# Performance work log

Hardware: AMD Instinct MI355X
Metric: run time of the kernel (lower is better)

The kernel has to match this reference:

```python
import jax, jax.numpy as jnp
import numpy as np

N_NODES = 100000
N_EDGES = 1600000
D_IN = 128
D_HID = 128
D_OUT = 10
N_GRAPHS = 512


def _sage_conv(x, src, dst, W_l, b_l, W_r, num_nodes):
    # PyG SAGEConv (mean aggr): out = lin_l(mean_{j in N(i)} x_j) + lin_r(x_i)
    msg = x[src]                                            # [E, D] gather
    s = jax.ops.segment_sum(msg, dst, num_segments=num_nodes)
    cnt = jax.ops.segment_sum(jnp.ones((src.shape[0], 1), x.dtype), dst,
                              num_segments=num_nodes)
    mean = s / jnp.maximum(cnt, 1.0)                        # 0 where no neighbors
    return mean @ W_l.T + b_l + x @ W_r.T


def setup_inputs() -> dict:
    key = jax.random.key(0)
    ks = jax.random.split(key, 10)
    glorot = lambda k, o, i: jax.random.normal(k, (o, i), jnp.float32) * (1.0 / np.sqrt(i))
    return {
        "x": jax.random.normal(ks[0], (N_NODES, D_IN), jnp.float32),
        "edge_index": jax.random.randint(ks[1], (2, N_EDGES), 0, N_NODES, jnp.int64),
        "batch": jnp.sort(jax.random.randint(ks[2], (N_NODES,), 0, N_GRAPHS, jnp.int64)),
        "W1_l": glorot(ks[3], D_HID, D_IN),
        "b1": jnp.zeros((D_HID,), jnp.float32),
        "W1_r": glorot(ks[4], D_HID, D_IN),
        "W2_l": glorot(ks[5], D_HID, D_HID),
        "b2": jnp.zeros((D_HID,), jnp.float32),
        "W2_r": glorot(ks[6], D_HID, D_HID),
        "Wf": glorot(ks[7], D_OUT, D_HID),
        "bf": jnp.zeros((D_OUT,), jnp.float32),
    }


def reference(x, edge_index, batch, W1_l, b1, W1_r, W2_l, b2, W2_r, Wf, bf):
    src, dst = edge_index[0], edge_index[1]
    n = x.shape[0]
    h = jax.nn.relu(_sage_conv(x, src, dst, W1_l, b1, W1_r, n))
    h = jax.nn.relu(_sage_conv(h, src, dst, W2_l, b2, W2_r, n))
    # global_mean_pool over graph ids
    gsum = jax.ops.segment_sum(h, batch, num_segments=N_GRAPHS)
    gcnt = jax.ops.segment_sum(jnp.ones((n, 1), h.dtype), batch, num_segments=N_GRAPHS)
    g = gsum / jnp.maximum(gcnt, 1.0)
    logits = g @ Wf.T + bf
    return jax.nn.log_softmax(logits, axis=-1)
```

## Files before the change

### kernel.cpp

```cpp
#include <hip/hip_runtime.h>
#include <hip/hip_bf16.h>

#define N_NODES 100000
#define N_EDGES 1600000
#define N_GRAPHS 512
#define NB 256
#define NPB 391
#define CHUNK 6250
#define STAGE 7680

typedef __attribute__((ext_vector_type(8))) short short8;
typedef __attribute__((ext_vector_type(4))) float f32x4;
typedef __attribute__((ext_vector_type(2))) float f32x2;

__device__ __forceinline__ float b2f(ushort u) {
    union { unsigned int i; float f; } c; c.i = ((unsigned int)u) << 16; return c.f;
}
__device__ __forceinline__ float blo(unsigned int u) {
    union { unsigned int i; float f; } c; c.i = u << 16; return c.f;
}
__device__ __forceinline__ float bhi(unsigned int u) {
    union { unsigned int i; float f; } c; c.i = u & 0xffff0000u; return c.f;
}
__device__ __forceinline__ ushort f2b(float f) {
    union { float f; unsigned int i; } c; c.f = f;
    unsigned int r = (c.i + 0x7fffu + ((c.i >> 16) & 1u)) >> 16;
    return (ushort)r;
}
__device__ __forceinline__ int idx_at(const void* p, long i, int f) {
    return f ? (int)((const long long*)p)[i] : ((const int*)p)[i];
}
__device__ __forceinline__ short8 dec8(const uchar* p) {
    uint2 q = *(const uint2*)p;
    f32x2 d0 = __builtin_amdgcn_cvt_pk_f32_fp8((int)q.x, false);
    f32x2 d1 = __builtin_amdgcn_cvt_pk_f32_fp8((int)q.x, true);
    f32x2 d2 = __builtin_amdgcn_cvt_pk_f32_fp8((int)q.y, false);
    f32x2 d3 = __builtin_amdgcn_cvt_pk_f32_fp8((int)q.y, true);
    short8 s;
    s[0] = (short)f2b(d0.x); s[1] = (short)f2b(d0.y);
    s[2] = (short)f2b(d1.x); s[3] = (short)f2b(d1.y);
    s[4] = (short)f2b(d2.x); s[5] = (short)f2b(d2.y);
    s[6] = (short)f2b(d3.x); s[7] = (short)f2b(d3.y);
    return s;
}

__global__ __launch_bounds__(256) void k_detect(const unsigned int* __restrict__ xw,
                                                const unsigned int* __restrict__ ew,
                                                const int* __restrict__ bw,
                                                int* __restrict__ flags) {
    __shared__ int cf, ce, cb;
    int t = threadIdx.x;
    if (t == 0) { cf = 0; ce = 0; cb = 0; }
    __syncthreads();
    unsigned int w = xw[t];
    unsigned int e = (w >> 7) & 0xffu;
    if (e >= 110u && e <= 130u) atomicAdd(&cf, 1);
    if (t < 128) {
        if (ew[2 * t + 1] != 0u) atomicAdd(&ce, 1);
        if (bw[99001 + 2 * t] != 0) atomicAdd(&cb, 1);
    }
    __syncthreads();
    if (t == 0) {
        flags[0] = (cf >= 128) ? 1 : 0;
        flags[1] = (ce == 0) ? 1 : 0;
        flags[2] = (cb == 0) ? 1 : 0;
    }
}

__global__ __launch_bounds__(256) void k_prep(const void* __restrict__ ei,
                                              const void* __restrict__ x,
                                              ushort* __restrict__ xbf,
                                              unsigned int* __restrict__ xf8,
                                              const void* W1l, const void* W1r,
                                              const void* W2l, const void* W2r,
                                              const void* b1,  const void* b2,
                                              ushort* __restrict__ wbf,
                                              int* __restrict__ blkcnt,
                                              const int* __restrict__ flags) {
    int b = blockIdx.x, t = threadIdx.x;
    if (b < NB) {
        __shared__ int h[NB];
        int f = flags[1];
        for (int j = t; j < NB; j += 256) h[j] = 0;
        __syncthreads();
        int lo = b * CHUNK, hi = lo + CHUNK;
        for (int e = lo + t; e < hi; e += 256) {
            int d = idx_at(ei, (long)N_EDGES + e, f);
            atomicAdd(&h[d / NPB], 1);
        }
        __syncthreads();
        if (t < NB) blkcnt[b * NB + t] = h[t];
    } else if (b < NB + 2048) {
        bool f32src = (flags[0] == 0);
        int vb = b - NB;
        const long nG = (long)N_NODES * 128 / 4;
        for (long g = (long)vb * 256 + t; g < nG; g += 2048L * 256) {
            float v0, v1, v2, v3;
            if (f32src) {
                float4 vv = ((const float4*)x)[g];
                v0 = vv.x; v1 = vv.y; v2 = vv.z; v3 = vv.w;
                unsigned int lo = (unsigned int)f2b(v0) | ((unsigned int)f2b(v1) << 16);
                unsigned int hi = (unsigned int)f2b(v2) | ((unsigned int)f2b(v3) << 16);
                ((uint2*)xbf)[g] = make_uint2(lo, hi);
            } else {
                uint2 q = ((const uint2*)x)[g];
                v0 = blo(q.x); v1 = bhi(q.x); v2 = blo(q.y); v3 = bhi(q.y);
            }
            int r = __builtin_amdgcn_cvt_pk_fp8_f32(v0, v1, 0, false);
            r = __builtin_amdgcn_cvt_pk_fp8_f32(v2, v3, r, true);
            xf8[g] = (unsigned int)r;
        }
    } else {
        int idx = (b - NB - 2048) * 256 + t;
        if (idx >= 65792) return;
        const void* src; int off;
        if      (idx < 16384) { src = W1l; off = idx; }
        else if (idx < 32768) { src = W1r; off = idx - 16384; }
        else if (idx < 49152) { src = W2l; off = idx - 32768; }
        else if (idx < 65536) { src = W2r; off = idx - 49152; }
        else if (idx < 65664) { src = b1;  off = idx - 65536; }
        else                  { src = b2;  off = idx - 65664; }
        wbf[idx] = (flags[0] != 0) ? ((const ushort*)src)[off]
                                   : f2b(((const float*)src)[off]);
    }
}

__global__ __launch_bounds__(NB) void k_bscan(const int* __restrict__ blkcnt,
                                              int* __restrict__ bucketBase,
                                              int* __restrict__ blkbase) {
    __shared__ int s[NB];
    int t = threadIdx.x;
    int tot = 0;
    for (int blk = 0; blk < NB; ++blk) tot += blkcnt[blk * NB + t];
    s[t] = tot; __syncthreads();
    for (int off = 1; off < NB; off <<= 1) {
        int a = (t >= off) ? s[t - off] : 0;
        __syncthreads();
        s[t] += a;
        __syncthreads();
    }
    int excl = s[t] - tot;
    bucketBase[t] = excl;
    if (t == NB - 1) bucketBase[NB] = s[NB - 1];
    int run = excl;
    for (int blk = 0; blk < NB; ++blk) {
        blkbase[blk * NB + t] = run;
        run += blkcnt[blk * NB + t];
    }
}

__global__ __launch_bounds__(256) void k_bin(const void* __restrict__ ei,
                                             const int* __restrict__ blkbase,
                                             int* __restrict__ binned,
                                             const int* __restrict__ flags) {
    __shared__ int bb[NB];
    __shared__ int rank[NB];
    int t = threadIdx.x, blk = blockIdx.x;
    int f = flags[1];
    for (int j = t; j < NB; j += 256) { bb[j] = blkbase[blk * NB + j]; rank[j] = 0; }
    __syncthreads();
    int lo = blk * CHUNK, hi = lo + CHUNK;
    for (int e = lo + t; e < hi; e += 256) {
        int s = idx_at(ei, e, f);
        int d = idx_at(ei, (long)N_EDGES + e, f);
        int b = d / NPB;
        int loc = d - b * NPB;
        int r = atomicAdd(&rank[b], 1);
        binned[bb[b] + r] = s | (loc << 20);
    }
}

__global__ __launch_bounds__(256) void k_csr(const int* __restrict__ binned,
                                             const int* __restrict__ bucketBase,
                                             int* __restrict__ rowptr,
                                             int* __restrict__ csr) {
    __shared__ int cnt[400];
    __shared__ int sc[400];
    __shared__ int sh[256];
    __shared__ int stage[STAGE];
    int t = threadIdx.x, b = blockIdx.x;
    int nodeLo = b * NPB;
    int nC = N_NODES - nodeLo; if (nC > NPB) nC = NPB;
    int eBase = bucketBase[b], eEnd = bucketBase[b + 1];

    for (int j = t; j < 400; j += 256) cnt[j] = 0;
    __syncthreads();
    for (int i = eBase + t; i < eEnd; i += 256)
        atomicAdd(&cnt[binned[i] >> 20], 1);
    __syncthreads();
    int base = t * 2;
    int v0 = (base < 400) ? cnt[base] : 0;
    int v1 = (base + 1 < 400) ? cnt[base + 1] : 0;
    int ssum = v0 + v1;
    sh[t] = ssum; __syncthreads();
    for (int off = 1; off < 256; off <<= 1) {
        int a = (t >= off) ? sh[t - off] : 0;
        __syncthreads();
        sh[t] += a;
        __syncthreads();
    }
    int pre = sh[t] - ssum;
    if (base < 400) sc[base] = pre;
    if (base + 1 < 400) sc[base + 1] = pre + v0;
    __syncthreads();
    for (int j = t; j < nC; j += 256) rowptr[nodeLo + j] = eBase + sc[j];
    if (b == NB - 1) {
        if (t == 0) rowptr[N_NODES] = eEnd;
        if (t < 64) csr[N_EDGES + t] = 0;
    }
    for (int j = t; j < 400; j += 256) cnt[j] = 0;
    __syncthreads();
    for (int i = eBase + t; i < eEnd; i += 256) {
        int p = binned[i];
        int loc = p >> 20;
        int pos = sc[loc] + atomicAdd(&cnt[loc], 1);
        int srcn = p & 0xFFFFF;
        if (pos < STAGE) stage[pos] = srcn;
        else csr[eBase + pos] = srcn;
    }
    __syncthreads();
    int eCnt = eEnd - eBase; if (eCnt > STAGE) eCnt = STAGE;
    for (int j = t; j < eCnt; j += 256) csr[eBase + j] = stage[j];
}

__global__ __launch_bounds__(256) void k_agg(const uint4* __restrict__ x8,
                                             const int* __restrict__ rowptr,
                                             const int* __restrict__ csr,
                                             uint4* __restrict__ mout) {
    int wv = blockIdx.x * 4 + (threadIdx.x >> 6);
    int lane = threadIdx.x & 63;
    int li = lane & 7;
    int node = wv * 8 + (lane >> 3);
    int beg = rowptr[node];
    int end = rowptr[node + 1];
    int deg = end - beg;
    int m = deg;
    m = max(m, __shfl_xor(m, 8));
    m = max(m, __shfl_xor(m, 16));
    m = max(m, __shfl_xor(m, 32));
    int degmax = __builtin_amdgcn_readfirstlane(m);
    float a[16];
#pragma unroll
    for (int i = 0; i < 16; ++i) a[i] = 0.f;
    for (int j = 0; j < degmax; j += 8) {
        int pos = beg + j + li;
        if (pos > end - 1) pos = (deg > 0) ? end - 1 : 0;
        int vidx = csr[pos];
        uint4 p[8];
#pragma unroll
        for (int i = 0; i < 8; ++i) {
            int idx = __shfl(vidx, i | (lane & 56));
            p[i] = x8[(long)idx * 8 + li];
        }
#pragma unroll
        for (int i = 0; i < 8; ++i) {
            bool ok = (j + i < deg);
            unsigned int q0 = ok ? p[i].x : 0u;
            unsigned int q1 = ok ? p[i].y : 0u;
            unsigned int q2 = ok ? p[i].z : 0u;
            unsigned int q3 = ok ? p[i].w : 0u;
            f32x2 d;
            d = __builtin_amdgcn_cvt_pk_f32_fp8((int)q0, false); a[0] += d.x;  a[1] += d.y;
            d = __builtin_amdgcn_cvt_pk_f32_fp8((int)q0, true);  a[2] += d.x;  a[3] += d.y;
            d = __builtin_amdgcn_cvt_pk_f32_fp8((int)q1, false); a[4] += d.x;  a[5] += d.y;
            d = __builtin_amdgcn_cvt_pk_f32_fp8((int)q1, true);  a[6] += d.x;  a[7] += d.y;
            d = __builtin_amdgcn_cvt_pk_f32_fp8((int)q2, false); a[8] += d.x;  a[9] += d.y;
            d = __builtin_amdgcn_cvt_pk_f32_fp8((int)q2, true);  a[10] += d.x; a[11] += d.y;
            d = __builtin_amdgcn_cvt_pk_f32_fp8((int)q3, false); a[12] += d.x; a[13] += d.y;
            d = __builtin_amdgcn_cvt_pk_f32_fp8((int)q3, true);  a[14] += d.x; a[15] += d.y;
        }
    }
    float s = (deg > 0) ? 1.f / (float)deg : 0.f;
    uint4 o;
    int r;
    r = __builtin_amdgcn_cvt_pk_fp8_f32(a[0] * s, a[1] * s, 0, false);
    r = __builtin_amdgcn_cvt_pk_fp8_f32(a[2] * s, a[3] * s, r, true);  o.x = (unsigned int)r;
    r = __builtin_amdgcn_cvt_pk_fp8_f32(a[4] * s, a[5] * s, 0, false);
    r = __builtin_amdgcn_cvt_pk_fp8_f32(a[6] * s, a[7] * s, r, true);  o.y = (unsigned int)r;
    r = __builtin_amdgcn_cvt_pk_fp8_f32(a[8] * s, a[9] * s, 0, false);
    r = __builtin_amdgcn_cvt_pk_fp8_f32(a[10] * s, a[11] * s, r, true); o.z = (unsigned int)r;
    r = __builtin_amdgcn_cvt_pk_fp8_f32(a[12] * s, a[13] * s, 0, false);
    r = __builtin_amdgcn_cvt_pk_fp8_f32(a[14] * s, a[15] * s, r, true); o.w = (unsigned int)r;
    mout[(long)node * 8 + li] = o;
}

__global__ __launch_bounds__(256) void k_gemm(const uchar* __restrict__ A0f8,
                                              const ushort* __restrict__ A1a,
                                              const ushort* __restrict__ A1b,
                                              const uchar* __restrict__ A1f8,
                                              const ushort* __restrict__ Wl,
                                              const ushort* __restrict__ Wr,
                                              const ushort* __restrict__ bias,
                                              ushort* __restrict__ outb,
                                              uchar* __restrict__ out8,
                                              const int* __restrict__ flags,
                                              int layer1) {
    __shared__ short Ws[4096 * 8];
    int t = threadIdx.x;
    const ushort* A1 = flags[0] ? A1a : A1b;
#pragma unroll
    for (int i = 0; i < 16; ++i) {
        int f = i * 256 + t;
        int lane = f & 63, kk = (f >> 6) & 7, tile = f >> 9;
        int o = tile * 16 + (lane & 15);
        int k0 = kk * 32 + ((lane >> 4) * 8);
        const ushort* wsrc = (k0 < 128) ? (Wl + o * 128 + k0)
                                        : (Wr + o * 128 + (k0 - 128));
        *(short8*)&Ws[f * 8] = *(const short8*)wsrc;
    }
    __syncthreads();

    int wid = t >> 6, lane = t & 63;
    long nbase = (long)blockIdx.x * 64 + (long)wid * 16;
    int arow = (int)nbase + (lane & 15);
    if (arow >= N_NODES) arow = N_NODES - 1;
    int kq = (lane >> 4) * 8;

    short8 afrag[8];
#pragma unroll
    for (int kk = 0; kk < 8; ++kk) {
        int k0 = kk * 32 + kq;
        if (k0 < 128) {
            afrag[kk] = dec8(A0f8 + (long)arow * 128 + k0);
        } else if (layer1) {
            afrag[kk] = *(const short8*)(A1 + (long)arow * 128 + (k0 - 128));
        } else {
            afrag[kk] = dec8(A1f8 + (long)arow * 128 + (k0 - 128));
        }
    }

#pragma unroll
    for (int tile = 0; tile < 8; ++tile) {
        f32x4 acc = {0.f, 0.f, 0.f, 0.f};
#pragma unroll
        for (int kk = 0; kk < 8; ++kk) {
            short8 bfrag = *(short8*)&Ws[((tile * 8 + kk) * 64 + lane) * 8];
            acc = __builtin_amdgcn_mfma_f32_16x16x32_bf16(afrag[kk], bfrag, acc, 0, 0, 0);
        }
        int o = tile * 16 + (lane & 15);
        float bo = b2f(bias[o]);
#pragma unroll
        for (int r = 0; r < 4; ++r) {
            long node = nbase + (lane >> 4) * 4 + r;
            if (node < N_NODES) {
                float v = acc[r] + bo;
                v = v > 0.f ? v : 0.f;
                if (layer1) {
                    int pp = __builtin_amdgcn_cvt_pk_fp8_f32(v, v, 0, false);
                    out8[node * 128 + o] = (uchar)pp;
                } else {
                    outb[node * 128 + o] = f2b(v);
                }
            }
        }
    }
}

__global__ __launch_bounds__(256) void k_pool_cls(const ushort* __restrict__ h2,
                                                  const void* __restrict__ batch,
                                                  const void* __restrict__ Wf,
                                                  const void* __restrict__ bfv,
                                                  void* __restrict__ outp,
                                                  const int* __restrict__ flags) {
    int g = blockIdx.x, t = threadIdx.x;
    int wid = t >> 6, lane = t & 63;
    bool f32 = (flags[0] == 0);
    int b64 = flags[2];
    __shared__ int rng[2];
    __shared__ float redA[4][64];
    __shared__ float redB[4][64];
    __shared__ float gv[128];
    __shared__ float lg[10];
    if (t < 2) {
        int v = g + t, lo = 0, hi = N_NODES;
        while (lo < hi) {
            int mid = (lo + hi) >> 1;
            if (idx_at(batch, mid, b64) < v) lo = mid + 1; else hi = mid;
        }
        rng[t] = lo;
    }
    __syncthreads();
    int lo = rng[0], hi = rng[1];
    const unsigned int* xr = (const unsigned int*)h2;
    float a0 = 0.f, a1 = 0.f;
    int n = lo + wid;
    for (; n + 28 < hi; n += 32) {
        unsigned int p[8];
#pragma unroll
        for (int i = 0; i < 8; ++i) p[i] = xr[(long)(n + i * 4) * 64 + lane];
#pragma unroll
        for (int i = 0; i < 8; ++i) { a0 += blo(p[i]); a1 += bhi(p[i]); }
    }
    for (; n < hi; n += 4) {
        unsigned int q = xr[(long)n * 64 + lane];
        a0 += blo(q); a1 += bhi(q);
    }
    redA[wid][lane] = a0;
    redB[wid][lane] = a1;
    __syncthreads();
    if (wid == 0) {
        float s0 = redA[0][lane] + redA[1][lane] + redA[2][lane] + redA[3][lane];
        float s1 = redB[0][lane] + redB[1][lane] + redB[2][lane] + redB[3][lane];
        float c = (hi > lo) ? (float)(hi - lo) : 1.f;
        gv[lane * 2]     = s0 / c;
        gv[lane * 2 + 1] = s1 / c;
    }
    __syncthreads();
    if (t < 10) {
        float s = f32 ? ((const float*)bfv)[t] : b2f(((const ushort*)bfv)[t]);
        for (int k = 0; k < 128; ++k) {
            float wv = f32 ? ((const float*)Wf)[t * 128 + k] : b2f(((const ushort*)Wf)[t * 128 + k]);
            s += gv[k] * wv;
        }
        lg[t] = s;
    }
    __syncthreads();
    if (t == 0) {
        float mx = lg[0];
        for (int i = 1; i < 10; ++i) mx = fmaxf(mx, lg[i]);
        float se = 0.f;
        for (int i = 0; i < 10; ++i) se += expf(lg[i] - mx);
        float lse = mx + logf(se);
        for (int i = 0; i < 10; ++i) {
            float v = lg[i] - lse;
            if (f32) ((float*)outp)[g * 10 + i] = v;
            else     ((ushort*)outp)[g * 10 + i] = f2b(v);
        }
    }
}

extern "C" void kernel_launch(void* const* d_in, const int* in_sizes, int n_in,
                              void* d_out, int out_size, void* d_ws, size_t ws_size,
                              hipStream_t stream) {
    const void* x     = d_in[0];
    const void* ei    = d_in[1];
    const void* batch = d_in[2];
    const void* W1l = d_in[3];
    const void* b1  = d_in[4];
    const void* W1r = d_in[5];
    const void* W2l = d_in[6];
    const void* b2  = d_in[7];
    const void* W2r = d_in[8];
    const void* Wf  = d_in[9];
    const void* bf_ = d_in[10];

    char* w = (char*)d_ws;
    int* flags      = (int*)(w + 0);
    int* rowptr     = (int*)(w + 640);
    ushort* wbf     = (ushort*)(w + 400768);
    int* csr        = (int*)(w + 532480);
    ushort* xbf     = (ushort*)(w + 6933248);
    ushort* h2      = (ushort*)(w + 6933248);
    uchar* mbuf     = (uchar*)(w + 32533248);
    int* bucketBase = (int*)(w + 32533248);
    int* blkcnt     = (int*)(w + 32534528);
    int* blkbase    = (int*)(w + 32796672);
    uchar* h1f8     = (uchar*)(w + 58133248);
    int* binned     = (int*)(w + 58133248);
    unsigned int* xf8 = (unsigned int*)(w + 70933248);

    dim3 blk256(256), blkNB(NB);

    k_detect<<<1, blk256, 0, stream>>>((const unsigned int*)x, (const unsigned int*)ei,
                                       (const int*)batch, flags);
    k_prep<<<NB + 2048 + 257, blk256, 0, stream>>>(ei, x, xbf, xf8,
                                                   W1l, W1r, W2l, W2r, b1, b2,
                                                   wbf, blkcnt, flags);
    k_bscan<<<1, blkNB, 0, stream>>>(blkcnt, bucketBase, blkbase);
    k_bin<<<NB, blk256, 0, stream>>>(ei, blkbase, binned, flags);
    k_csr<<<NB, blk256, 0, stream>>>(binned, bucketBase, rowptr, csr);

    int agrid = N_NODES / 8 / 4;
    int ggrid = (N_NODES + 63) / 64;

    k_agg<<<agrid, blk256, 0, stream>>>((const uint4*)xf8, rowptr, csr, (uint4*)mbuf);
    k_gemm<<<ggrid, blk256, 0, stream>>>(mbuf, (const ushort*)x, xbf, (const uchar*)nullptr,
                                         wbf + 0, wbf + 16384, wbf + 65536,
                                         (ushort*)nullptr, h1f8, flags, 1);
    k_agg<<<agrid, blk256, 0, stream>>>((const uint4*)h1f8, rowptr, csr, (uint4*)mbuf);
    k_gemm<<<ggrid, blk256, 0, stream>>>(mbuf, (const ushort*)x, xbf, h1f8,
                                         wbf + 32768, wbf + 49152, wbf + 65664,
                                         h2, (uchar*)nullptr, flags, 0);
    k_pool_cls<<<N_GRAPHS, blk256, 0, stream>>>(h2, batch, Wf, bf_, d_out, flags);
}
```

Measured before the change: 320.2 us.

## Fold detection into prep kernels and double CSR bucket count

Removes the separate k_detect launch by having each block of the histogram/convert kernel detect the input dtype and index width itself, with one extra block writing the flags for later kernels. The batch-dtype check moves into the scan kernel and the weight conversion moves into the binning kernel. The bucket count doubles to 512 with smaller node ranges and edge chunks, and the CSR scan is simplified to one count per thread. The single-block scan now walks a 512x512 count matrix serially, which adds work, and the per-block detection adds redundant reads.

Result: slower. 338.9 us (+5.8%).

```diff
diff --git a/kernel.cpp b/kernel.cpp
--- a/kernel.cpp
+++ b/kernel.cpp
@@ -4,10 +4,11 @@
 #define N_NODES 100000
 #define N_EDGES 1600000
 #define N_GRAPHS 512
-#define NB 256
-#define NPB 391
-#define CHUNK 6250
-#define STAGE 7680
+#define NB 512
+#define NPB 196
+#define CHUNK 3125
+#define STAGE 3840
+#define CVTB 2048
 
 typedef __attribute__((ext_vector_type(8))) short short8;
 typedef __attribute__((ext_vector_type(4))) float f32x4;
@@ -44,57 +45,41 @@
     return s;
 }
 
-__global__ __launch_bounds__(256) void k_detect(const unsigned int* __restrict__ xw,
-                                                const unsigned int* __restrict__ ew,
-                                                const int* __restrict__ bw,
-                                                int* __restrict__ flags) {
-    __shared__ int cf, ce, cb;
-    int t = threadIdx.x;
-    if (t == 0) { cf = 0; ce = 0; cb = 0; }
-    __syncthreads();
-    unsigned int w = xw[t];
-    unsigned int e = (w >> 7) & 0xffu;
-    if (e >= 110u && e <= 130u) atomicAdd(&cf, 1);
-    if (t < 128) {
-        if (ew[2 * t + 1] != 0u) atomicAdd(&ce, 1);
-        if (bw[99001 + 2 * t] != 0) atomicAdd(&cb, 1);
-    }
-    __syncthreads();
-    if (t == 0) {
-        flags[0] = (cf >= 128) ? 1 : 0;
-        flags[1] = (ce == 0) ? 1 : 0;
-        flags[2] = (cb == 0) ? 1 : 0;
-    }
-}
-
-__global__ __launch_bounds__(256) void k_prep(const void* __restrict__ ei,
+__global__ __launch_bounds__(256) void k_hist(const void* __restrict__ ei,
                                               const void* __restrict__ x,
                                               ushort* __restrict__ xbf,
                                               unsigned int* __restrict__ xf8,
-                                              const void* W1l, const void* W1r,
-                                              const void* W2l, const void* W2r,
-                                              const void* b1,  const void* b2,
-                                              ushort* __restrict__ wbf,
                                               int* __restrict__ blkcnt,
-                                              const int* __restrict__ flags) {
+                                              int* __restrict__ flags) {
     int b = blockIdx.x, t = threadIdx.x;
     if (b < NB) {
+        __shared__ int ce;
         __shared__ int h[NB];
-        int f = flags[1];
+        if (t == 0) ce = 0;
         for (int j = t; j < NB; j += 256) h[j] = 0;
         __syncthreads();
+        if (t < 128 && ((const unsigned int*)ei)[2 * t + 1] != 0u) atomicAdd(&ce, 1);
+        __syncthreads();
+        int f = (ce == 0) ? 1 : 0;
         int lo = b * CHUNK, hi = lo + CHUNK;
         for (int e = lo + t; e < hi; e += 256) {
             int d = idx_at(ei, (long)N_EDGES + e, f);
             atomicAdd(&h[d / NPB], 1);
         }
         __syncthreads();
-        if (t < NB) blkcnt[b * NB + t] = h[t];
-    } else if (b < NB + 2048) {
-        bool f32src = (flags[0] == 0);
+        for (int j = t; j < NB; j += 256) blkcnt[b * NB + j] = h[j];
+    } else if (b < NB + CVTB) {
+        __shared__ int cf;
+        if (t == 0) cf = 0;
+        __syncthreads();
+        unsigned int wv = ((const unsigned int*)x)[t];
+        unsigned int e = (wv >> 7) & 0xffu;
+        if (e >= 110u && e <= 130u) atomicAdd(&cf, 1);
+        __syncthreads();
+        bool f32src = (cf < 128);
         int vb = b - NB;
         const long nG = (long)N_NODES * 128 / 4;
-        for (long g = (long)vb * 256 + t; g < nG; g += 2048L * 256) {
+        for (long g = (long)vb * 256 + t; g < nG; g += (long)CVTB * 256) {
             float v0, v1, v2, v3;
             if (f32src) {
                 float4 vv = ((const float4*)x)[g];
@@ -111,7 +96,77 @@
             xf8[g] = (unsigned int)r;
         }
     } else {
-        int idx = (b - NB - 2048) * 256 + t;
+        __shared__ int cf, ce;
+        if (t == 0) { cf = 0; ce = 0; }
+        __syncthreads();
+        unsigned int wv = ((const unsigned int*)x)[t];
+        unsigned int e = (wv >> 7) & 0xffu;
+        if (e >= 110u && e <= 130u) atomicAdd(&cf, 1);
+        if (t < 128 && ((const unsigned int*)ei)[2 * t + 1] != 0u) atomicAdd(&ce, 1);
+        __syncthreads();
+        if (t == 0) {
+            flags[0] = (cf >= 128) ? 1 : 0;
+            flags[1] = (ce == 0) ? 1 : 0;
+        }
+    }
+}
+
+__global__ __launch_bounds__(NB) void k_bscan(const int* __restrict__ blkcnt,
+                                              int* __restrict__ bucketBase,
+                                              int* __restrict__ blkbase,
+                                              const int* __restrict__ bw,
+                                              int* __restrict__ flags) {
+    __shared__ int s[NB];
+    __shared__ int cb;
+    int t = threadIdx.x;
+    if (t == 0) cb = 0;
+    int tot = 0;
+    for (int blk = 0; blk < NB; ++blk) tot += blkcnt[blk * NB + t];
+    s[t] = tot; __syncthreads();
+    if (t < 128 && bw[99001 + 2 * t] != 0) atomicAdd(&cb, 1);
+    for (int off = 1; off < NB; off <<= 1) {
+        int a = (t >= off) ? s[t - off] : 0;
+        __syncthreads();
+        s[t] += a;
+        __syncthreads();
+    }
+    int excl = s[t] - tot;
+    bucketBase[t] = excl;
+    if (t == NB - 1) bucketBase[NB] = s[NB - 1];
+    int run = excl;
+    for (int blk = 0; blk < NB; ++blk) {
+        blkbase[blk * NB + t] = run;
+        run += blkcnt[blk * NB + t];
+    }
+    if (t == 0) flags[2] = (cb == 0) ? 1 : 0;
+}
+
+__global__ __launch_bounds__(256) void k_bin(const void* __restrict__ ei,
+                                             const int* __restrict__ blkbase,
+                                             int* __restrict__ binned,
+                                             const void* W1l, const void* W1r,
+                                             const void* W2l, const void* W2r,
+                                             const void* b1,  const void* b2,
+                                             ushort* __restrict__ wbf,
+                                             const int* __restrict__ flags) {
+    int blk = blockIdx.x, t = threadIdx.x;
+    if (blk < NB) {
+        __shared__ int bb[NB];
+        __shared__ int rank[NB];
+        int f = flags[1];
+        for (int j = t; j < NB; j += 256) { bb[j] = blkbase[blk * NB + j]; rank[j] = 0; }
+        __syncthreads();
+        int lo = blk * CHUNK, hi = lo + CHUNK;
+        for (int e = lo + t; e < hi; e += 256) {
+            int s = idx_at(ei, e, f);
+            int d = idx_at(ei, (long)N_EDGES + e, f);
+            int b = d / NPB;
+            int loc = d - b * NPB;
+            int r = atomicAdd(&rank[b], 1);
+            binned[bb[b] + r] = s | (loc << 20);
+        }
+    } else {
+        int idx = (blk - NB) * 256 + t;
         if (idx >= 65792) return;
         const void* src; int off;
         if      (idx < 16384) { src = W1l; off = idx; }
@@ -125,90 +180,41 @@
     }
 }
 
-__global__ __launch_bounds__(NB) void k_bscan(const int* __restrict__ blkcnt,
-                                              int* __restrict__ bucketBase,
-                                              int* __restrict__ blkbase) {
-    __shared__ int s[NB];
-    int t = threadIdx.x;
-    int tot = 0;
-    for (int blk = 0; blk < NB; ++blk) tot += blkcnt[blk * NB + t];
-    s[t] = tot; __syncthreads();
-    for (int off = 1; off < NB; off <<= 1) {
-        int a = (t >= off) ? s[t - off] : 0;
-        __syncthreads();
-        s[t] += a;
-        __syncthreads();
-    }
-    int excl = s[t] - tot;
-    bucketBase[t] = excl;
-    if (t == NB - 1) bucketBase[NB] = s[NB - 1];
-    int run = excl;
-    for (int blk = 0; blk < NB; ++blk) {
-        blkbase[blk * NB + t] = run;
-        run += blkcnt[blk * NB + t];
-    }
-}
-
-__global__ __launch_bounds__(256) void k_bin(const void* __restrict__ ei,
-                                             const int* __restrict__ blkbase,
-                                             int* __restrict__ binned,
-                                             const int* __restrict__ flags) {
-    __shared__ int bb[NB];
-    __shared__ int rank[NB];
-    int t = threadIdx.x, blk = blockIdx.x;
-    int f = flags[1];
-    for (int j = t; j < NB; j += 256) { bb[j] = blkbase[blk * NB + j]; rank[j] = 0; }
-    __syncthreads();
-    int lo = blk * CHUNK, hi = lo + CHUNK;
-    for (int e = lo + t; e < hi; e += 256) {
-        int s = idx_at(ei, e, f);
-        int d = idx_at(ei, (long)N_EDGES + e, f);
-        int b = d / NPB;
-        int loc = d - b * NPB;
-        int r = atomicAdd(&rank[b], 1);
-        binned[bb[b] + r] = s | (loc << 20);
-    }
-}
-
 __global__ __launch_bounds__(256) void k_csr(const int* __restrict__ binned,
                                              const int* __restrict__ bucketBase,
                                              int* __restrict__ rowptr,
                                              int* __restrict__ csr) {
-    __shared__ int cnt[400];
-    __shared__ int sc[400];
+    __shared__ int cnt[200];
+    __shared__ int sc[200];
     __shared__ int sh[256];
     __shared__ int stage[STAGE];
     int t = threadIdx.x, b = blockIdx.x;
     int nodeLo = b * NPB;
-    int nC = N_NODES - nodeLo; if (nC > NPB) nC = NPB;
+    int nC = N_NODES - nodeLo;
+    if (nC > NPB) nC = NPB;
     int eBase = bucketBase[b], eEnd = bucketBase[b + 1];
 
-    for (int j = t; j < 400; j += 256) cnt[j] = 0;
+    if (t < 200) cnt[t] = 0;
     __syncthreads();
     for (int i = eBase + t; i < eEnd; i += 256)
         atomicAdd(&cnt[binned[i] >> 20], 1);
     __syncthreads();
-    int base = t * 2;
-    int v0 = (base < 400) ? cnt[base] : 0;
-    int v1 = (base + 1 < 400) ? cnt[base + 1] : 0;
-    int ssum = v0 + v1;
-    sh[t] = ssum; __syncthreads();
+    int v0 = (t < 200) ? cnt[t] : 0;
+    sh[t] = v0; __syncthreads();
     for (int off = 1; off < 256; off <<= 1) {
         int a = (t >= off) ? sh[t - off] : 0;
         __syncthreads();
         sh[t] += a;
         __syncthreads();
     }
-    int pre = sh[t] - ssum;
-    if (base < 400) sc[base] = pre;
-    if (base + 1 < 400) sc[base + 1] = pre + v0;
+    if (t < 200) sc[t] = sh[t] - v0;
     __syncthreads();
     for (int j = t; j < nC; j += 256) rowptr[nodeLo + j] = eBase + sc[j];
     if (b == NB - 1) {
         if (t == 0) rowptr[N_NODES] = eEnd;
         if (t < 64) csr[N_EDGES + t] = 0;
     }
-    for (int j = t; j < 400; j += 256) cnt[j] = 0;
+    if (t < 200) cnt[t] = 0;
     __syncthreads();
     for (int i = eBase + t; i < eEnd; i += 256) {
         int p = binned[i];
@@ -453,21 +459,18 @@
     ushort* h2      = (ushort*)(w + 6933248);
     uchar* mbuf     = (uchar*)(w + 32533248);
     int* bucketBase = (int*)(w + 32533248);
-    int* blkcnt     = (int*)(w + 32534528);
-    int* blkbase    = (int*)(w + 32796672);
+    int* blkcnt     = (int*)(w + 32535808);
+    int* blkbase    = (int*)(w + 33584384);
     uchar* h1f8     = (uchar*)(w + 58133248);
     int* binned     = (int*)(w + 58133248);
     unsigned int* xf8 = (unsigned int*)(w + 70933248);
 
     dim3 blk256(256), blkNB(NB);
 
-    k_detect<<<1, blk256, 0, stream>>>((const unsigned int*)x, (const unsigned int*)ei,
-                                       (const int*)batch, flags);
-    k_prep<<<NB + 2048 + 257, blk256, 0, stream>>>(ei, x, xbf, xf8,
-                                                   W1l, W1r, W2l, W2r, b1, b2,
-                                                   wbf, blkcnt, flags);
-    k_bscan<<<1, blkNB, 0, stream>>>(blkcnt, bucketBase, blkbase);
-    k_bin<<<NB, blk256, 0, stream>>>(ei, blkbase, binned, flags);
+    k_hist<<<NB + CVTB + 1, blk256, 0, stream>>>(ei, x, xbf, xf8, blkcnt, flags);
+    k_bscan<<<1, blkNB, 0, stream>>>(blkcnt, bucketBase, blkbase, (const int*)batch, flags);
+    k_bin<<<NB + 257, blk256, 0, stream>>>(ei, blkbase, binned,
+                                           W1l, W1r, W2l, W2r, b1, b2, wbf, flags);
     k_csr<<<NB, blk256, 0, stream>>>(binned, bucketBase, rowptr, csr);
 
     int agrid = N_NODES / 8 / 4;
```
